# Kernel tuning notes

Hardware: AMD Instinct MI355X
Metric: run time of the kernel (lower is better)

Reference implementation:

```python
import jax, jax.numpy as jnp
import numpy as np

D = 16        # d_model
DFF = 128     # ffn hidden
H_NN = 128    # pairwise-MLP hidden
RES = 1.0     # res_ratio (undefined global in source; standard residual)
EPS = 1e-6


def setup_inputs() -> dict:
    key = jax.random.key(0)
    ks = jax.random.split(key, 16)
    B, G, L = 8, 1, 256
    def n(k, shape, s=0.05):
        return jax.random.normal(k, shape, jnp.float32) * s
    return dict(
        x=jax.random.normal(ks[0], (B, G, L, D), jnp.float32),
        mask=jnp.zeros((B, G, L, L), jnp.float32),
        wq=n(ks[1], (D, D)), bq=jnp.zeros((D,), jnp.float32),
        wk=n(ks[2], (D, D)), bk=jnp.zeros((D,), jnp.float32),
        wv=n(ks[3], (D, D)), bv=jnp.zeros((D,), jnp.float32),
        wo=n(ks[4], (D, D)), bo=jnp.zeros((D,), jnp.float32),
        nn_w1=n(ks[5], (2 * D, H_NN)), nn_b1=jnp.zeros((H_NN,), jnp.float32),
        nn_w2=n(ks[6], (H_NN, 1)), nn_b2=jnp.zeros((1,), jnp.float32),
        f1=n(ks[7], (D, DFF)), f1b=jnp.zeros((DFF,), jnp.float32),
        f2=n(ks[8], (DFF, D)), f2b=jnp.zeros((D,), jnp.float32),
        g1=jnp.ones((D,), jnp.float32), be1=jnp.zeros((D,), jnp.float32),
        g2=jnp.ones((D,), jnp.float32), be2=jnp.zeros((D,), jnp.float32),
    )


def _layernorm(x, g, b):
    m = jnp.mean(x, -1, keepdims=True)
    v = jnp.var(x, -1, keepdims=True)
    return (x - m) * jax.lax.rsqrt(v + EPS) * g + b


def reference(x, mask, wq, bq, wk, bk, wv, bv, wo, bo,
              nn_w1, nn_b1, nn_w2, nn_b2,
              f1, f1b, f2, f2b, g1, be1, g2, be2):
    # projections: (B,G,L,D)
    q = x @ wq + bq
    k = x @ wk + bk
    v = x @ wv + bv
    # pairwise relation-network attention.
    # NN(concat([q_i, k_j])) first layer splits as q_i @ W1[:D] + k_j @ W1[D:]
    w1q, w1k = nn_w1[:D], nn_w1[D:]
    w2 = nn_w2[:, 0]
    qa = q @ w1q  # (B,G,L,H)
    kb = k @ w1k
    h1 = jax.nn.relu(qa[:, :, :, None, :] + kb[:, :, None, :, :] + nn_b1)  # (B,G,Lq,Lk,H)
    logits = jnp.einsum('bgijh,h->bgij', h1, w2) + nn_b2[0]
    # make_sym: NN(concat([k_j, q_i])) -> k_j @ W1[:D] + q_i @ W1[D:]
    ka = k @ w1q
    qb = q @ w1k
    h2 = jax.nn.relu(qb[:, :, :, None, :] + ka[:, :, None, :, :] + nn_b1)
    logits = logits + jnp.einsum('bgijh,h->bgij', h2, w2) + nn_b2[0]
    logits = logits + mask * -1e9
    attn = jax.nn.softmax(logits, axis=-1)          # (B,G,Lq,Lk)
    ctx = jnp.einsum('bgij,bgjd->bgid', attn, v)    # (B,G,L,D)
    attn_out = ctx @ wo + bo
    out1 = _layernorm(RES * x + (2.0 - RES) * attn_out, g1, be1)
    ffn = jax.nn.relu(out1 @ f1 + f1b) @ f2 + f2b
    out2 = _layernorm(RES * out1 + (2.0 - RES) * ffn, g2, be2)
    return out2
```

## Files before the change

### kernel.cpp

```cpp
#include <hip/hip_runtime.h>
#include <hip/hip_bf16.h>

typedef __hip_bfloat16 bf16;

constexpr int DIM  = 16;
constexpr int HNN  = 128;
constexpr int SEQ  = 256;
constexpr int BAT  = 8;
constexpr int ROWS = BAT * SEQ;
constexpr int QT   = 4;
constexpr int NBLK = ROWS / QT;

__device__ __forceinline__ bool is_f32(const void* g1) {
  return ((const unsigned*)g1)[0] == 0x3F800000u;
}
__device__ __forceinline__ float ld(const void* p, long i, bool f32) {
  return f32 ? ((const float*)p)[i]
             : __bfloat162float(((const bf16*)p)[i]);
}

__global__ __launch_bounds__(128) void prep_kernel(
    const void* __restrict__ x,
    const void* __restrict__ wq, const void* __restrict__ bq,
    const void* __restrict__ wk, const void* __restrict__ bk,
    const void* __restrict__ wv, const void* __restrict__ bv,
    const void* __restrict__ nn_w1, const void* __restrict__ nn_b1,
    const void* __restrict__ nn_w2, const void* __restrict__ g1flag,
    float* __restrict__ qa, float* __restrict__ qb,
    float* __restrict__ kkT, float* __restrict__ vT, float* __restrict__ w2f)
{
  const bool f32 = is_f32(g1flag);
  const int row = blockIdx.x;
  const int tid = threadIdx.x;
  __shared__ float xs[DIM], qs[DIM], ks[DIM], vs[DIM];

  if (tid < DIM) xs[tid] = ld(x, (long)row * DIM + tid, f32);
  __syncthreads();

  if (tid < 3 * DIM) {
    const int which = tid >> 4, d = tid & 15;
    const void* w  = (which == 0) ? wq : (which == 1) ? wk : wv;
    const void* bb = (which == 0) ? bq : (which == 1) ? bk : bv;
    float acc = ld(bb, d, f32);
    #pragma unroll
    for (int e = 0; e < DIM; e++) acc += xs[e] * ld(w, e * DIM + d, f32);
    if (which == 0) qs[d] = acc;
    else if (which == 1) ks[d] = acc;
    else vs[d] = acc;
  }
  __syncthreads();

  float qw1q = 0.f, qw1k = 0.f, kw1q = 0.f, kw1k = 0.f;
  #pragma unroll
  for (int d = 0; d < DIM; d++) {
    float a = ld(nn_w1, d * HNN + tid, f32);
    float b = ld(nn_w1, (DIM + d) * HNN + tid, f32);
    qw1q += qs[d] * a;  qw1k += qs[d] * b;
    kw1q += ks[d] * a;  kw1k += ks[d] * b;
  }
  const float b1 = ld(nn_b1, tid, f32);
  qa[row * HNN + tid] = qw1q;
  qb[row * HNN + tid] = qw1k;
  ((float2*)kkT)[((size_t)(tid >> 1) * ROWS + row) * 2 + (tid & 1)] =
      make_float2(kw1k + b1, kw1q + b1);
  if (tid < DIM) vT[tid * ROWS + row] = vs[tid];
  if (row == 0) w2f[tid] = ld(nn_w2, tid, f32);
}

__global__ __launch_bounds__(256) void attn_kernel(
    const void* __restrict__ x,  const void* __restrict__ mask,
    const void* __restrict__ wo, const void* __restrict__ bo,
    const void* __restrict__ nn_b2,
    const void* __restrict__ f1, const void* __restrict__ f1b,
    const void* __restrict__ f2, const void* __restrict__ f2b,
    const void* __restrict__ g1, const void* __restrict__ be1,
    const void* __restrict__ g2, const void* __restrict__ be2,
    const float* __restrict__ qa, const float* __restrict__ qb,
    const float* __restrict__ kkT, const float* __restrict__ vT,
    const float* __restrict__ w2f,
    void* __restrict__ out)
{
  const bool f32 = is_f32(g1);
  const int blk  = blockIdx.x;
  const int bi   = blk >> 6;
  const int i0   = (blk & 63) * QT;
  const int t    = threadIdx.x;
  const int j    = t;
  const int col  = bi * SEQ + j;
  const int lane = t & 63, wv = t >> 6;

  __shared__ float pb[QT][SEQ];
  __shared__ float vbufT[SEQ][DIM + 1];
  __shared__ float wred[2][QT][4];
  __shared__ float ctxs[QT][DIM];
  __shared__ float tmpA[QT][DIM];
  __shared__ float tmpB[QT][DIM];
  __shared__ float hids[QT][HNN];

  #pragma unroll
  for (int d = 0; d < DIM; ++d) vbufT[j][d] = vT[d * ROWS + col];

  const float* qaB = qa + (size_t)(bi * SEQ + i0) * HNN;
  const float* qbB = qb + (size_t)(bi * SEQ + i0) * HNN;
  float acc[QT] = {0.f, 0.f, 0.f, 0.f};
  #pragma unroll 2
  for (int hp = 0; hp < HNN / 2; ++hp) {
    const float4 kk = ((const float4*)kkT)[(size_t)hp * ROWS + col];
    const float w0 = w2f[2 * hp], w1 = w2f[2 * hp + 1];
    #pragma unroll
    for (int ii = 0; ii < QT; ++ii) {
      const float* qai = qaB + ii * HNN;
      const float* qbi = qbB + ii * HNN;
      float s0 = fmaxf(qai[2 * hp]     + kk.x, 0.f) + fmaxf(qbi[2 * hp]     + kk.y, 0.f);
      float s1 = fmaxf(qai[2 * hp + 1] + kk.z, 0.f) + fmaxf(qbi[2 * hp + 1] + kk.w, 0.f);
      acc[ii] = fmaf(w0, s0, acc[ii]);
      acc[ii] = fmaf(w1, s1, acc[ii]);
    }
  }

  const float b2v = ld(nn_b2, 0, f32);
  float la[QT], e[QT];
  #pragma unroll
  for (int ii = 0; ii < QT; ++ii)
    la[ii] = acc[ii] + 2.f * b2v
           + ld(mask, ((size_t)bi * SEQ + (i0 + ii)) * SEQ + j, f32) * -1e9f;

  #pragma unroll
  for (int ii = 0; ii < QT; ++ii) {
    float m = la[ii];
    #pragma unroll
    for (int off = 32; off > 0; off >>= 1) m = fmaxf(m, __shfl_xor(m, off, 64));
    if (lane == 0) wred[0][ii][wv] = m;
  }
  __syncthreads();
  #pragma unroll
  for (int ii = 0; ii < QT; ++ii) {
    const float mx = fmaxf(fmaxf(wred[0][ii][0], wred[0][ii][1]),
                           fmaxf(wred[0][ii][2], wred[0][ii][3]));
    const float ev = __expf(la[ii] - mx);
    e[ii] = ev;
    float s = ev;
    #pragma unroll
    for (int off = 32; off > 0; off >>= 1) s += __shfl_xor(s, off, 64);
    if (lane == 0) wred[1][ii][wv] = s;
    pb[ii][j] = ev;
  }
  __syncthreads();

  if (t < QT * DIM) {
    const int ii = t >> 4, d = t & 15;
    float s = 0.f;
    #pragma unroll 8
    for (int jj = 0; jj < SEQ; ++jj) s += pb[ii][jj] * vbufT[jj][d];
    const float inv = 1.f / (wred[1][ii][0] + wred[1][ii][1] +
                             wred[1][ii][2] + wred[1][ii][3]);
    ctxs[ii][d] = s * inv;
  }
  __syncthreads();

  if (t < QT * DIM) {
    const int ii = t >> 4, d = t & 15;
    float ao = ld(bo, d, f32);
    #pragma unroll
    for (int dd = 0; dd < DIM; ++dd) ao += ctxs[ii][dd] * ld(wo, dd * DIM + d, f32);
    tmpA[ii][d] = ld(x, ((size_t)(bi * SEQ + i0 + ii)) * DIM + d, f32) + ao;
  }
  __syncthreads();

  if (t < QT * DIM) {
    const int ii = t >> 4, d = t & 15;
    float m = 0.f;
    #pragma unroll
    for (int dd = 0; dd < DIM; ++dd) m += tmpA[ii][dd];
    m *= (1.f / DIM);
    float v = 0.f;
    #pragma unroll
    for (int dd = 0; dd < DIM; ++dd) { float z = tmpA[ii][dd] - m; v += z * z; }
    v *= (1.f / DIM);
    tmpB[ii][d] = (tmpA[ii][d] - m) * rsqrtf(v + 1e-6f) * ld(g1, d, f32)
                + ld(be1, d, f32);
  }
  __syncthreads();

  #pragma unroll
  for (int p = 0; p < 2; ++p) {
    const int ii = (t >> 7) + 2 * p;
    const int h  = t & 127;
    float a = ld(f1b, h, f32);
    #pragma unroll
    for (int dd = 0; dd < DIM; ++dd) a += tmpB[ii][dd] * ld(f1, dd * HNN + h, f32);
    hids[ii][h] = fmaxf(a, 0.f);
  }
  __syncthreads();

  if (t < QT * DIM) {
    const int ii = t >> 4, d = t & 15;
    float a = ld(f2b, d, f32);
    for (int h = 0; h < HNN; ++h) a += hids[ii][h] * ld(f2, h * DIM + d, f32);
    tmpA[ii][d] = tmpB[ii][d] + a;
  }
  __syncthreads();

  if (t < QT * DIM) {
    const int ii = t >> 4, d = t & 15;
    float m = 0.f;
    #pragma unroll
    for (int dd = 0; dd < DIM; ++dd) m += tmpA[ii][dd];
    m *= (1.f / DIM);
    float v = 0.f;
    #pragma unroll
    for (int dd = 0; dd < DIM; ++dd) { float z = tmpA[ii][dd] - m; v += z * z; }
    v *= (1.f / DIM);
    const float val = (tmpA[ii][d] - m) * rsqrtf(v + 1e-6f) * ld(g2, d, f32)
                    + ld(be2, d, f32);
    const long oidx = ((long)(bi * SEQ + i0 + ii)) * DIM + d;
    if (f32) ((float*)out)[oidx] = val;
    else     ((bf16*)out)[oidx] = __float2bfloat16(val);
  }
}

extern "C" void kernel_launch(void* const* d_in, const int* in_sizes, int n_in,
                              void* d_out, int out_size, void* d_ws, size_t ws_size,
                              hipStream_t stream) {
  const void* x     = d_in[0];
  const void* mask  = d_in[1];
  const void* wq    = d_in[2];
  const void* bq    = d_in[3];
  const void* wk    = d_in[4];
  const void* bk    = d_in[5];
  const void* wv    = d_in[6];
  const void* bv    = d_in[7];
  const void* wo    = d_in[8];
  const void* bo    = d_in[9];
  const void* nn_w1 = d_in[10];
  const void* nn_b1 = d_in[11];
  const void* nn_w2 = d_in[12];
  const void* nn_b2 = d_in[13];
  const void* f1    = d_in[14];
  const void* f1b   = d_in[15];
  const void* f2    = d_in[16];
  const void* f2b   = d_in[17];
  const void* g1    = d_in[18];
  const void* be1   = d_in[19];
  const void* g2    = d_in[20];
  const void* be2   = d_in[21];

  float* qa  = (float*)d_ws;
  float* qb  = qa  + (size_t)ROWS * HNN;
  float* kkT = qb  + (size_t)ROWS * HNN;
  float* vT  = kkT + (size_t)ROWS * HNN * 2;
  float* w2f = vT  + (size_t)DIM * ROWS;

  prep_kernel<<<ROWS, 128, 0, stream>>>(x, wq, bq, wk, bk, wv, bv, nn_w1, nn_b1,
                                        nn_w2, g1, qa, qb, kkT, vT, w2f);
  attn_kernel<<<NBLK, 256, 0, stream>>>(x, mask, wo, bo, nn_b2,
                                        f1, f1b, f2, f2b, g1, be1, g2, be2,
                                        qa, qb, kkT, vT, w2f, d_out);
}
```

Before: 138.0 us.

## Split attention hidden dimension across four thread groups with 1024-thread blocks

Raises the attention block from 256 to 1024 threads. Each group of 256 threads handles a quarter of the pairwise-MLP hidden dimension, and the partial logits are reduced through shared memory. The context and FFN second-layer matvecs are spread over all threads as 16-way partial sums, replacing the old 64-thread serial loops. This gives more parallelism per query tile and shorter serial tails, at the cost of extra shared memory, barriers and an idle 3/4 of threads during softmax.

```diff
diff --git a/kernel.cpp b/kernel.cpp
--- a/kernel.cpp
+++ b/kernel.cpp
@@ -67,7 +67,7 @@
   if (row == 0) w2f[tid] = ld(nn_w2, tid, f32);
 }
 
-__global__ __launch_bounds__(256) void attn_kernel(
+__global__ __launch_bounds__(1024) void attn_kernel(
     const void* __restrict__ x,  const void* __restrict__ mask,
     const void* __restrict__ wo, const void* __restrict__ bo,
     const void* __restrict__ nn_b2,
@@ -81,30 +81,38 @@
     void* __restrict__ out)
 {
   const bool f32 = is_f32(g1);
-  const int blk  = blockIdx.x;
-  const int bi   = blk >> 6;
-  const int i0   = (blk & 63) * QT;
-  const int t    = threadIdx.x;
-  const int j    = t;
-  const int col  = bi * SEQ + j;
-  const int lane = t & 63, wv = t >> 6;
+  const int blk = blockIdx.x;
+  const int bi  = blk >> 6;
+  const int i0  = (blk & 63) * QT;
+  const int t   = threadIdx.x;
+  const int g   = t >> 8;
+  const int j   = t & 255;
+  const int col = bi * SEQ + j;
 
   __shared__ float pb[QT][SEQ];
   __shared__ float vbufT[SEQ][DIM + 1];
+  __shared__ float part[4][QT][SEQ];
   __shared__ float wred[2][QT][4];
   __shared__ float ctxs[QT][DIM];
   __shared__ float tmpA[QT][DIM];
   __shared__ float tmpB[QT][DIM];
   __shared__ float hids[QT][HNN];
 
-  #pragma unroll
-  for (int d = 0; d < DIM; ++d) vbufT[j][d] = vT[d * ROWS + col];
+  float* pf = &part[0][0][0];
+
+  {
+    const int d0 = g * 4;
+    #pragma unroll
+    for (int d = 0; d < 4; ++d)
+      vbufT[j][d0 + d] = vT[(d0 + d) * ROWS + col];
+  }
 
   const float* qaB = qa + (size_t)(bi * SEQ + i0) * HNN;
   const float* qbB = qb + (size_t)(bi * SEQ + i0) * HNN;
   float acc[QT] = {0.f, 0.f, 0.f, 0.f};
-  #pragma unroll 2
-  for (int hp = 0; hp < HNN / 2; ++hp) {
+  const int hp0 = g * 16;
+  #pragma unroll 4
+  for (int hp = hp0; hp < hp0 + 16; ++hp) {
     const float4 kk = ((const float4*)kkT)[(size_t)hp * ROWS + col];
     const float w0 = w2f[2 * hp], w1 = w2f[2 * hp + 1];
     #pragma unroll
@@ -117,41 +125,55 @@
       acc[ii] = fmaf(w1, s1, acc[ii]);
     }
   }
-
-  const float b2v = ld(nn_b2, 0, f32);
-  float la[QT], e[QT];
   #pragma unroll
-  for (int ii = 0; ii < QT; ++ii)
-    la[ii] = acc[ii] + 2.f * b2v
-           + ld(mask, ((size_t)bi * SEQ + (i0 + ii)) * SEQ + j, f32) * -1e9f;
-
-  #pragma unroll
-  for (int ii = 0; ii < QT; ++ii) {
-    float m = la[ii];
-    #pragma unroll
-    for (int off = 32; off > 0; off >>= 1) m = fmaxf(m, __shfl_xor(m, off, 64));
-    if (lane == 0) wred[0][ii][wv] = m;
-  }
-  __syncthreads();
-  #pragma unroll
-  for (int ii = 0; ii < QT; ++ii) {
-    const float mx = fmaxf(fmaxf(wred[0][ii][0], wred[0][ii][1]),
-                           fmaxf(wred[0][ii][2], wred[0][ii][3]));
-    const float ev = __expf(la[ii] - mx);
-    e[ii] = ev;
-    float s = ev;
-    #pragma unroll
-    for (int off = 32; off > 0; off >>= 1) s += __shfl_xor(s, off, 64);
-    if (lane == 0) wred[1][ii][wv] = s;
-    pb[ii][j] = ev;
-  }
-  __syncthreads();
-
-  if (t < QT * DIM) {
-    const int ii = t >> 4, d = t & 15;
+  for (int ii = 0; ii < QT; ++ii) part[g][ii][j] = acc[ii];
+  __syncthreads();
+
+  const int lane = t & 63, wvi = t >> 6;
+  float la[QT];
+  if (t < 256) {
+    const float b2v = ld(nn_b2, 0, f32);
+    #pragma unroll
+    for (int ii = 0; ii < QT; ++ii) {
+      la[ii] = part[0][ii][j] + part[1][ii][j] + part[2][ii][j] + part[3][ii][j]
+             + 2.f * b2v
+             + ld(mask, ((size_t)bi * SEQ + (i0 + ii)) * SEQ + j, f32) * -1e9f;
+      float m = la[ii];
+      #pragma unroll
+      for (int off = 32; off > 0; off >>= 1) m = fmaxf(m, __shfl_xor(m, off, 64));
+      if (lane == 0) wred[0][ii][wvi] = m;
+    }
+  }
+  __syncthreads();
+  if (t < 256) {
+    #pragma unroll
+    for (int ii = 0; ii < QT; ++ii) {
+      const float mx = fmaxf(fmaxf(wred[0][ii][0], wred[0][ii][1]),
+                             fmaxf(wred[0][ii][2], wred[0][ii][3]));
+      const float ev = __expf(la[ii] - mx);
+      float s = ev;
+      #pragma unroll
+      for (int off = 32; off > 0; off >>= 1) s += __shfl_xor(s, off, 64);
+      if (lane == 0) wred[1][ii][wvi] = s;
+      pb[ii][j] = ev;
+    }
+  }
+  __syncthreads();
+
+  {
+    const int ii = g, d = t & 15, c = (t >> 4) & 15;
     float s = 0.f;
-    #pragma unroll 8
-    for (int jj = 0; jj < SEQ; ++jj) s += pb[ii][jj] * vbufT[jj][d];
+    #pragma unroll
+    for (int jj = 0; jj < 16; ++jj)
+      s += pb[ii][c * 16 + jj] * vbufT[c * 16 + jj][d];
+    pf[ii * 256 + d * 16 + c] = s;
+  }
+  __syncthreads();
+  if (t < QT * DIM) {
+    const int ii = t >> 4, d = t & 15;
+    float s = 0.f;
+    #pragma unroll
+    for (int c = 0; c < 16; ++c) s += pf[ii * 256 + d * 16 + c];
     const float inv = 1.f / (wred[1][ii][0] + wred[1][ii][1] +
                              wred[1][ii][2] + wred[1][ii][3]);
     ctxs[ii][d] = s * inv;
@@ -182,10 +204,8 @@
   }
   __syncthreads();
 
-  #pragma unroll
-  for (int p = 0; p < 2; ++p) {
-    const int ii = (t >> 7) + 2 * p;
-    const int h  = t & 127;
+  if (t < QT * HNN) {
+    const int ii = t >> 7, h = t & 127;
     float a = ld(f1b, h, f32);
     #pragma unroll
     for (int dd = 0; dd < DIM; ++dd) a += tmpB[ii][dd] * ld(f1, dd * HNN + h, f32);
@@ -193,10 +213,22 @@
   }
   __syncthreads();
 
+  {
+    const int ii = g, d = t & 15, c = (t >> 4) & 15;
+    float a = 0.f;
+    #pragma unroll
+    for (int hh = 0; hh < 8; ++hh) {
+      const int h = c * 8 + hh;
+      a += hids[ii][h] * ld(f2, h * DIM + d, f32);
+    }
+    pf[ii * 256 + d * 16 + c] = a;
+  }
+  __syncthreads();
   if (t < QT * DIM) {
     const int ii = t >> 4, d = t & 15;
     float a = ld(f2b, d, f32);
-    for (int h = 0; h < HNN; ++h) a += hids[ii][h] * ld(f2, h * DIM + d, f32);
+    #pragma unroll
+    for (int c = 0; c < 16; ++c) a += pf[ii * 256 + d * 16 + c];
     tmpA[ii][d] = tmpB[ii][d] + a;
   }
   __syncthreads();
@@ -253,7 +285,7 @@
 
   prep_kernel<<<ROWS, 128, 0, stream>>>(x, wq, bq, wk, bk, wv, bv, nn_w1, nn_b1,
                                         nn_w2, g1, qa, qb, kkT, vT, w2f);
-  attn_kernel<<<NBLK, 256, 0, stream>>>(x, mask, wo, bo, nn_b2,
-                                        f1, f1b, f2, f2b, g1, be1, g2, be2,
-                                        qa, qb, kkT, vT, w2f, d_out);
-}
+  attn_kernel<<<NBLK, 1024, 0, stream>>>(x, mask, wo, bo, nn_b2,
+                                         f1, f1b, f2, f2b, g1, be1, g2, be2,
+                                         qa, qb, kkT, vT, w2f, d_out);
+}
```

Result: slower. 141.5 us (+2.6%).
